# Optimization experiments

Hardware: AMD Instinct MI355X
Metric: run time of the kernel (lower is better)

The kernel has to match this reference:

```python
import jax, jax.numpy as jnp
import numpy as np

EMBED_DIM = 1024
NUM_HEADS = 16
HEAD_DIM = EMBED_DIM // NUM_HEADS
SCALE = HEAD_DIM ** -0.5


def setup_inputs() -> dict:
    key = jax.random.key(0)
    k_x, k_qkv_w, k_qkv_b, k_p_w, k_p_b = jax.random.split(key, 5)
    B, N, C = 4, 2048, EMBED_DIM
    std = C ** -0.5
    return {
        "x": jax.random.normal(k_x, (B, N, C), dtype=jnp.float32),
        "qkv_w": jax.random.normal(k_qkv_w, (C, 3 * C), dtype=jnp.float32) * std,
        "qkv_b": jax.random.normal(k_qkv_b, (3 * C,), dtype=jnp.float32) * 0.02,
        "proj_w": jax.random.normal(k_p_w, (C, C), dtype=jnp.float32) * std,
        "proj_b": jax.random.normal(k_p_b, (C,), dtype=jnp.float32) * 0.02,
    }


def reference(x, qkv_w, qkv_b, proj_w, proj_b):
    B, N, C = x.shape
    H, D = NUM_HEADS, HEAD_DIM
    # fused QKV projection: [B, N, 3C] -> [3, B, H, N, D]
    qkv = (x @ qkv_w + qkv_b).reshape(B, N, 3, H, D).transpose(2, 0, 3, 1, 4)
    q, k, v = qkv[0], qkv[1], qkv[2]
    # explicit N x N attention (faithful to the original, no fused SDPA)
    attn = jnp.einsum("bhqd,bhkd->bhqk", q, k) * SCALE
    attn = jax.nn.softmax(attn, axis=-1)
    out = jnp.einsum("bhqk,bhkd->bhqd", attn, v)  # [B, H, N, D]
    out = out.transpose(0, 2, 1, 3).reshape(B, N, C)
    return out @ proj_w + proj_b
```

## Files before the change

### kernel.cpp

```cpp
#include <hip/hip_runtime.h>
#include <hip/hip_bf16.h>

typedef __bf16 bf16x8 __attribute__((ext_vector_type(8)));
typedef __bf16 bf16x4 __attribute__((ext_vector_type(4)));
typedef float  f32x4  __attribute__((ext_vector_type(4)));

#define MFMA_BF16(a, b, c) __builtin_amdgcn_mfma_f32_16x16x32_bf16((a), (b), (c), 0, 0, 0)

typedef const __attribute__((address_space(1))) void* gas_ptr;
typedef __attribute__((address_space(3))) void* las_ptr;

__device__ __forceinline__ void gload_lds16(const void* g, void* l) {
    __builtin_amdgcn_global_load_lds((gas_ptr)g, (las_ptr)l, 16, 0, 0);
}

__device__ __forceinline__ float fast_exp2(float x) {
#if __has_builtin(__builtin_amdgcn_exp2f)
    return __builtin_amdgcn_exp2f(x);
#else
    return __builtin_exp2f(x);
#endif
}

#define LOG2E 1.44269504088896f
#define QSCALE 0.1803368801111204f

__global__ __launch_bounds__(256) void prep_fused(const float* __restrict__ x,
                                                  const float* __restrict__ qkv_w,
                                                  const float* __restrict__ proj_w,
                                                  __bf16* __restrict__ Xb,
                                                  __bf16* __restrict__ Wqkvt,
                                                  __bf16* __restrict__ Wpt) {
    const int b = blockIdx.x;
    if (b < 8192) {
        int i = b * 256 + threadIdx.x;
        float4 v = ((const float4*)x)[i];
        bf16x4 o = {(__bf16)v.x, (__bf16)v.y, (__bf16)v.z, (__bf16)v.w};
        ((bf16x4*)Xb)[i] = o;
        return;
    }
    __shared__ float t[32][33];
    const float* in;
    __bf16* out;
    int R, C, bx, by;
    if (b < 11264) {
        int bb = b - 8192;
        in = qkv_w; out = Wqkvt; R = 1024; C = 3072;
        bx = (bb % 96) * 32; by = (bb / 96) * 32;
    } else {
        int bb = b - 11264;
        in = proj_w; out = Wpt; R = 1024; C = 1024;
        bx = (bb % 32) * 32; by = (bb / 32) * 32;
    }
    const int tx = threadIdx.x & 31, ty = threadIdx.x >> 5;
    int xcol = bx + tx;
    for (int j = ty; j < 32; j += 8)
        t[j][tx] = in[(size_t)(by + j) * C + xcol];
    __syncthreads();
    int x2 = by + tx;
    for (int j = ty; j < 32; j += 8)
        out[(size_t)(bx + j) * R + x2] = (__bf16)t[tx][j];
}

template <int MODE>
__global__ __launch_bounds__(256) void gemm_bt(const __bf16* __restrict__ A,
                                               const __bf16* __restrict__ Bt,
                                               const float* __restrict__ bias,
                                               float* __restrict__ outp,
                                               __bf16* __restrict__ Qp,
                                               __bf16* __restrict__ Kp,
                                               __bf16* __restrict__ Vp,
                                               int M, int Nn, int K) {
    __shared__ __align__(16) __bf16 SA[3][4096];
    __shared__ __align__(16) __bf16 SB[3][4096];
    const int tid = threadIdx.x, lane = tid & 63, w = tid >> 6;
    const int wr = w >> 1, wc = w & 1;
    const int nbx = Nn >> 7;
    const int nwg = (M >> 7) * nbx;
    const int cpx = nwg >> 3;
    const int id = blockIdx.x;
    const int nid = (id & 7) * cpx + (id >> 3);
    const int row0 = (nid / nbx) * 128, col0 = (nid % nbx) * 128;
    const __bf16* Ag = A + (size_t)row0 * K;
    const __bf16* Bg = Bt + (size_t)col0 * K;
    const int lr = lane >> 2;
    const int srcc = ((lane & 3) ^ ((lane >> 3) & 3)) * 8;
    const int frow = lane & 15, fq = lane >> 4;
    const int rdoff = (fq ^ ((frow >> 1) & 3)) * 8;
    f32x4 acc[4][4];
    for (int i = 0; i < 4; ++i)
        for (int j = 0; j < 4; ++j) acc[i][j] = (f32x4)0.f;

    auto stage = [&](int t, __bf16* Ad, __bf16* Bd) {
#pragma unroll
        for (int it = 0; it < 2; ++it) {
            int ci = 2 * w + it;
            gload_lds16(Ag + (size_t)(ci * 16 + lr) * K + t * 32 + srcc, Ad + ci * 512);
            gload_lds16(Bg + (size_t)(ci * 16 + lr) * K + t * 32 + srcc, Bd + ci * 512);
        }
    };

    const int NK = K >> 5;
    __bf16 *cA = SA[0], *cB = SB[0];
    __bf16 *nA = SA[1], *nB = SB[1];
    __bf16 *sA = SA[2], *sB = SB[2];
    stage(0, cA, cB);
    stage(1, nA, nB);

    for (int t = 0; t < NK; ++t) {
        if (t < NK - 1)
            asm volatile("s_waitcnt vmcnt(4)" ::: "memory");
        else
            asm volatile("s_waitcnt vmcnt(0)" ::: "memory");
        __builtin_amdgcn_s_barrier();
        if (t + 2 < NK) stage(t + 2, sA, sB);

        bf16x8 af[4], bf[4];
#pragma unroll
        for (int i = 0; i < 4; ++i)
            af[i] = *(const bf16x8*)&cA[(wr * 64 + i * 16 + frow) * 32 + rdoff];
#pragma unroll
        for (int j = 0; j < 4; ++j)
            bf[j] = *(const bf16x8*)&cB[(wc * 64 + j * 16 + frow) * 32 + rdoff];
#pragma unroll
        for (int i = 0; i < 4; ++i)
#pragma unroll
            for (int j = 0; j < 4; ++j) acc[i][j] = MFMA_BF16(af[i], bf[j], acc[i][j]);

        __bf16* tA = cA; cA = nA; nA = sA; sA = tA;
        __bf16* tB = cB; cB = nB; nB = sB; sB = tB;
    }

    for (int i = 0; i < 4; ++i) {
        int rbase = row0 + wr * 64 + i * 16 + fq * 4;
        for (int j = 0; j < 4; ++j) {
            int c = col0 + wc * 64 + j * 16 + frow;
            float bv = bias[c];
            if (MODE == 0) {
                int which = c >> 10;
                int h = (c >> 6) & 15;
                int d = c & 63;
                if (which == 2) {
                    int b = rbase >> 11, n = rbase & 2047;
                    int nph = (n & ~31) | (((n >> 2) & 3) << 3) | (((n >> 4) & 1) << 2) |
                              (n & 3);
                    bf16x4 vv = {(__bf16)(acc[i][j][0] + bv), (__bf16)(acc[i][j][1] + bv),
                                 (__bf16)(acc[i][j][2] + bv), (__bf16)(acc[i][j][3] + bv)};
                    *(bf16x4*)&Vp[(size_t)(((b << 4) + h) * 64 + d) * 2048 + nph] = vv;
                } else {
                    for (int rg = 0; rg < 4; ++rg) {
                        int rr = rbase + rg;
                        int b = rr >> 11, n = rr & 2047;
                        float v = acc[i][j][rg] + bv;
                        if (which == 0)
                            Qp[(size_t)(((b << 4) + h) * 2048 + n) * 64 + d] =
                                (__bf16)(v * QSCALE);
                        else
                            Kp[(size_t)(((b << 4) + h) * 2048 + n) * 64 + d] = (__bf16)v;
                    }
                }
            } else {
                for (int rg = 0; rg < 4; ++rg)
                    outp[(size_t)(rbase + rg) * Nn + c] = acc[i][j][rg] + bv;
            }
        }
    }
}

__global__ __launch_bounds__(256, 4) void flash_attn8(const __bf16* __restrict__ Q,
                                                      const __bf16* __restrict__ K,
                                                      const __bf16* __restrict__ Vt,
                                                      __bf16* __restrict__ O) {
    __shared__ __align__(16) __bf16 Kts[2][4096];
    __shared__ __align__(16) __bf16 Vts[2][4096];
    const int tid = threadIdx.x, lane = tid & 63, w = tid >> 6;
    const int frow = lane & 15, fq = lane >> 4;
    const int id = blockIdx.x;
    const int nid = (id & 7) * 128 + (id >> 3);
    const int bh = nid >> 4;
    const int q0 = (nid & 15) * 128;
    const __bf16* Qg = Q + ((size_t)bh * 2048 + q0 + w * 32) * 64;
    const __bf16* Kb = K + (size_t)bh * 2048 * 64;
    const __bf16* Vb = Vt + (size_t)bh * 64 * 2048;

    bf16x8 qf[2][2];
#pragma unroll
    for (int nt = 0; nt < 2; ++nt)
#pragma unroll
        for (int ks = 0; ks < 2; ++ks)
            qf[nt][ks] = *(const bf16x8*)(Qg + (nt * 16 + frow) * 64 + ks * 32 + fq * 8);

    bf16x8 ones;
#pragma unroll
    for (int i = 0; i < 8; ++i) ones[i] = (__bf16)1.0f;

    f32x4 acc[2][4];
#pragma unroll
    for (int i = 0; i < 2; ++i)
#pragma unroll
        for (int j = 0; j < 4; ++j) acc[i][j] = (f32x4)0.f;
    f32x4 acc_l[2];
#pragma unroll
    for (int i = 0; i < 2; ++i) acc_l[i] = (f32x4)0.f;

    const int s_r16 = lane >> 2;
    const int s_c8 = (((lane & 3) ^ ((lane >> 3) & 3))) * 8;

    auto stage = [&](int kt, __bf16* Kd, __bf16* Vd) {
#pragma unroll
        for (int it = 0; it < 2; ++it) {
            int ci = 2 * w + it;
            int ks = ci >> 2;
            int r16 = (ci & 3) * 16 + s_r16;
            gload_lds16(Kb + (size_t)(kt * 64 + r16) * 64 + ks * 32 + s_c8, Kd + ci * 512);
            gload_lds16(Vb + (size_t)r16 * 2048 + kt * 64 + ks * 32 + s_c8, Vd + ci * 512);
        }
    };

    stage(0, Kts[0], Vts[0]);

    const int key = (frow >> 1) & 3;
    const int slot = (fq ^ key) * 8;

    auto body = [&](int kt, const __bf16* Kc, const __bf16* Vc, __bf16* Kn, __bf16* Vn) {
        __syncthreads();
        if (kt < 31) stage(kt + 1, Kn, Vn);

#pragma unroll
        for (int ph = 0; ph < 2; ++ph) {
            bf16x8 pf[2];
#pragma unroll
            for (int mi = 0; mi < 2; ++mi) {
                int mt = ph * 2 + mi;
                bf16x8 a0 = *(const bf16x8*)&Kc[(mt * 16 + frow) * 32 + slot];
                bf16x8 a1 = *(const bf16x8*)&Kc[2048 + (mt * 16 + frow) * 32 + slot];
#pragma unroll
                for (int nt = 0; nt < 2; ++nt) {
                    __builtin_amdgcn_s_setprio(1);
                    f32x4 s = MFMA_BF16(a0, qf[nt][0], (f32x4)0.f);
                    s = MFMA_BF16(a1, qf[nt][1], s);
                    __builtin_amdgcn_s_setprio(0);
                    pf[nt][mi * 4 + 0] = (__bf16)fast_exp2(s[0]);
                    pf[nt][mi * 4 + 1] = (__bf16)fast_exp2(s[1]);
                    pf[nt][mi * 4 + 2] = (__bf16)fast_exp2(s[2]);
                    pf[nt][mi * 4 + 3] = (__bf16)fast_exp2(s[3]);
                }
            }

            __builtin_amdgcn_s_setprio(1);
#pragma unroll
            for (int nt = 0; nt < 4; ++nt) {
                bf16x8 vf = *(const bf16x8*)&Vc[ph * 2048 + (nt * 16 + frow) * 32 + slot];
                acc[0][nt] = MFMA_BF16(pf[0], vf, acc[0][nt]);
                acc[1][nt] = MFMA_BF16(pf[1], vf, acc[1][nt]);
            }
            acc_l[0] = MFMA_BF16(pf[0], ones, acc_l[0]);
            acc_l[1] = MFMA_BF16(pf[1], ones, acc_l[1]);
            __builtin_amdgcn_s_setprio(0);
        }
    };

    for (int kt = 0; kt < 32; kt += 2) {
        body(kt, Kts[0], Vts[0], Kts[1], Vts[1]);
        body(kt + 1, Kts[1], Vts[1], Kts[0], Vts[0]);
    }

    const int b = bh >> 4, h = bh & 15;
#pragma unroll
    for (int mq = 0; mq < 2; ++mq)
#pragma unroll
        for (int r = 0; r < 4; ++r) {
            float linv = 1.0f / acc_l[mq][r];
            int qg = q0 + w * 32 + mq * 16 + fq * 4 + r;
            __bf16* orow = O + ((size_t)(b * 2048 + qg)) * 1024 + h * 64 + frow;
#pragma unroll
            for (int nt = 0; nt < 4; ++nt)
                orow[nt * 16] = (__bf16)(acc[mq][nt][r] * linv);
        }
}

extern "C" void kernel_launch(void* const* d_in, const int* in_sizes, int n_in,
                              void* d_out, int out_size, void* d_ws, size_t ws_size,
                              hipStream_t stream) {
    const float* x      = (const float*)d_in[0];
    const float* qkv_w  = (const float*)d_in[1];
    const float* qkv_b  = (const float*)d_in[2];
    const float* proj_w = (const float*)d_in[3];
    const float* proj_b = (const float*)d_in[4];
    float* out = (float*)d_out;

    char* ws = (char*)d_ws;
    __bf16* Xb     = (__bf16*)(ws);
    __bf16* Wqkvt  = (__bf16*)(ws + 16777216);
    __bf16* Wpt    = (__bf16*)(ws + 23068672);
    __bf16* Qb     = (__bf16*)(ws + 25165824);
    __bf16* Kb     = (__bf16*)(ws + 41943040);
    __bf16* Vtb    = (__bf16*)(ws + 58720256);
    __bf16* AttnOut = Xb;

    prep_fused<<<12288, 256, 0, stream>>>(x, qkv_w, proj_w, Xb, Wqkvt, Wpt);

    gemm_bt<0><<<1536, 256, 0, stream>>>(Xb, Wqkvt, qkv_b, nullptr,
                                         Qb, Kb, Vtb, 8192, 3072, 1024);

    flash_attn8<<<1024, 256, 0, stream>>>(Qb, Kb, Vtb, AttnOut);

    gemm_bt<1><<<512, 256, 0, stream>>>(AttnOut, Wpt, proj_b, out,
                                        nullptr, nullptr, nullptr, 8192, 1024, 1024);
}
```

Before: 261.1 us.

## Software-pipeline LDS fragment reads with MFMA in the GEMM main loop

The GEMM K-loop is unrolled by two and given two register sets for the A/B fragments. The next tile's fragments are read from LDS before the current tile's MFMAs issue, and the global-to-LDS stage for tile t+2 is issued before the barrier instead of after it. MFMA blocks are wrapped in s_setprio raises, and launch bounds now request three blocks per CU. The aim is to hide LDS read latency behind matrix math, at the cost of more fragment registers and a loop that assumes an even number of K-steps.

```diff
diff --git a/kernel.cpp b/kernel.cpp
--- a/kernel.cpp
+++ b/kernel.cpp
@@ -63,14 +63,14 @@
 }
 
 template <int MODE>
-__global__ __launch_bounds__(256) void gemm_bt(const __bf16* __restrict__ A,
-                                               const __bf16* __restrict__ Bt,
-                                               const float* __restrict__ bias,
-                                               float* __restrict__ outp,
-                                               __bf16* __restrict__ Qp,
-                                               __bf16* __restrict__ Kp,
-                                               __bf16* __restrict__ Vp,
-                                               int M, int Nn, int K) {
+__global__ __launch_bounds__(256, 3) void gemm_bt(const __bf16* __restrict__ A,
+                                                  const __bf16* __restrict__ Bt,
+                                                  const float* __restrict__ bias,
+                                                  float* __restrict__ outp,
+                                                  __bf16* __restrict__ Qp,
+                                                  __bf16* __restrict__ Kp,
+                                                  __bf16* __restrict__ Vp,
+                                                  int M, int Nn, int K) {
     __shared__ __align__(16) __bf16 SA[3][4096];
     __shared__ __align__(16) __bf16 SB[3][4096];
     const int tid = threadIdx.x, lane = tid & 63, w = tid >> 6;
@@ -90,6 +90,7 @@
     f32x4 acc[4][4];
     for (int i = 0; i < 4; ++i)
         for (int j = 0; j < 4; ++j) acc[i][j] = (f32x4)0.f;
+    bf16x8 afA[4], bfA[4], afB[4], bfB[4];
 
     auto stage = [&](int t, __bf16* Ad, __bf16* Bd) {
 #pragma unroll
@@ -99,36 +100,57 @@
             gload_lds16(Bg + (size_t)(ci * 16 + lr) * K + t * 32 + srcc, Bd + ci * 512);
         }
     };
+    auto readfr = [&](bf16x8* af, bf16x8* bf, const __bf16* cA, const __bf16* cB) {
+#pragma unroll
+        for (int i = 0; i < 4; ++i)
+            af[i] = *(const bf16x8*)&cA[(wr * 64 + i * 16 + frow) * 32 + rdoff];
+#pragma unroll
+        for (int j = 0; j < 4; ++j)
+            bf[j] = *(const bf16x8*)&cB[(wc * 64 + j * 16 + frow) * 32 + rdoff];
+    };
+    auto mfma16 = [&](const bf16x8* af, const bf16x8* bf) {
+        __builtin_amdgcn_s_setprio(1);
+#pragma unroll
+        for (int i = 0; i < 4; ++i)
+#pragma unroll
+            for (int j = 0; j < 4; ++j) acc[i][j] = MFMA_BF16(af[i], bf[j], acc[i][j]);
+        __builtin_amdgcn_s_setprio(0);
+    };
 
     const int NK = K >> 5;
-    __bf16 *cA = SA[0], *cB = SB[0];
-    __bf16 *nA = SA[1], *nB = SB[1];
-    __bf16 *sA = SA[2], *sB = SB[2];
-    stage(0, cA, cB);
-    stage(1, nA, nB);
-
-    for (int t = 0; t < NK; ++t) {
-        if (t < NK - 1)
+    __bf16 *a0 = SA[0], *a1 = SA[1], *a2 = SA[2];
+    __bf16 *b0 = SB[0], *b1 = SB[1], *b2 = SB[2];
+    stage(0, a0, b0);
+    stage(1, a1, b1);
+    asm volatile("s_waitcnt vmcnt(4)" ::: "memory");
+    __builtin_amdgcn_s_barrier();
+    readfr(afA, bfA, a0, b0);
+
+    for (int t = 0; t < NK; t += 2) {
+        if (t + 2 < NK) stage(t + 2, a2, b2);
+        if (t + 2 < NK)
             asm volatile("s_waitcnt vmcnt(4)" ::: "memory");
         else
             asm volatile("s_waitcnt vmcnt(0)" ::: "memory");
+        asm volatile("s_waitcnt lgkmcnt(0)" ::: "memory");
         __builtin_amdgcn_s_barrier();
-        if (t + 2 < NK) stage(t + 2, sA, sB);
-
-        bf16x8 af[4], bf[4];
-#pragma unroll
-        for (int i = 0; i < 4; ++i)
-            af[i] = *(const bf16x8*)&cA[(wr * 64 + i * 16 + frow) * 32 + rdoff];
-#pragma unroll
-        for (int j = 0; j < 4; ++j)
-            bf[j] = *(const bf16x8*)&cB[(wc * 64 + j * 16 + frow) * 32 + rdoff];
-#pragma unroll
-        for (int i = 0; i < 4; ++i)
-#pragma unroll
-            for (int j = 0; j < 4; ++j) acc[i][j] = MFMA_BF16(af[i], bf[j], acc[i][j]);
-
-        __bf16* tA = cA; cA = nA; nA = sA; sA = tA;
-        __bf16* tB = cB; cB = nB; nB = sB; sB = tB;
+        readfr(afB, bfB, a1, b1);
+        mfma16(afA, bfA);
+        __bf16* tp;
+        tp = a0; a0 = a1; a1 = a2; a2 = tp;
+        tp = b0; b0 = b1; b1 = b2; b2 = tp;
+
+        if (t + 3 < NK) stage(t + 3, a2, b2);
+        if (t + 3 < NK)
+            asm volatile("s_waitcnt vmcnt(4)" ::: "memory");
+        else if (t + 2 < NK)
+            asm volatile("s_waitcnt vmcnt(0)" ::: "memory");
+        asm volatile("s_waitcnt lgkmcnt(0)" ::: "memory");
+        __builtin_amdgcn_s_barrier();
+        if (t + 2 < NK) readfr(afA, bfA, a1, b1);
+        mfma16(afB, bfB);
+        tp = a0; a0 = a1; a1 = a2; a2 = tp;
+        tp = b0; b0 = b1; b1 = b2; b2 = tp;
     }
 
     for (int i = 0; i < 4; ++i) {
```

New measurement: 257.3 us, median of 2. Within noise of the previous version (-1.5%).
